# Optimization experiments

Hardware: AMD Instinct MI355X
Metric: run time of the kernel (lower is better)

Reference implementation:

```python
import jax, jax.numpy as jnp
import numpy as np

BLUR = 0.05
P = 2
EPS_FINAL = BLUR ** P          # geomloss: eps = blur**p = 0.0025
DIAMETER = 2.0                 # max cosine cost magnitude
SCALING = 0.5                  # geomloss default; eps decays by scaling**p per step
N_FINAL_ITERS = 4              # extra balancing iterations at the final eps


def eps_schedule():
    eps_list = []
    e = DIAMETER ** P
    while e > EPS_FINAL:
        eps_list.append(e)
        e = e * (SCALING ** P)
    eps_list.extend([EPS_FINAL] * N_FINAL_ITERS)
    return eps_list


def cosine_cost(a, b):
    # a: (N, D), b: (M, D) -> (N, M) cost = 1 - cos_sim
    an = a / (jnp.linalg.norm(a, axis=1, keepdims=True) + 1e-12)
    bn = b / (jnp.linalg.norm(b, axis=1, keepdims=True) + 1e-12)
    return 1.0 - an @ bn.T


def softmin(C, pot, log_w, eps):
    # -eps * LSE_j( log_w + (pot_j - C_ij)/eps ) ; C: (N, M), pot: (M,)
    return -eps * jax.nn.logsumexp(log_w + (pot[None, :] - C) / eps, axis=1)


def sinkhorn_divergence(Cxy, Cxx, Cyy):
    N, M = Cxy.shape
    log_a = -jnp.log(jnp.asarray(N, dtype=Cxy.dtype))  # uniform weights
    log_b = -jnp.log(jnp.asarray(M, dtype=Cxy.dtype))
    sg = jax.lax.stop_gradient
    # Sinkhorn iterations run on detached costs (geomloss envelope-theorem trick)
    Cxy_s, Cxx_s, Cyy_s = sg(Cxy), sg(Cxx), sg(Cyy)
    f = jnp.zeros((N,), Cxy.dtype)
    g = jnp.zeros((M,), Cxy.dtype)
    fxx = jnp.zeros((N,), Cxy.dtype)
    gyy = jnp.zeros((M,), Cxy.dtype)
    for eps in eps_schedule():
        # symmetric (debiasing) potentials: averaged fixed-point update
        fxx = 0.5 * (fxx + softmin(Cxx_s, fxx, log_a, eps))
        gyy = 0.5 * (gyy + softmin(Cyy_s, gyy, log_b, eps))
        # cross potentials: simultaneous (Jacobi) update
        f, g = softmin(Cxy_s, g, log_b, eps), softmin(Cxy_s.T, f, log_a, eps)
    # final extrapolation step with gradients flowing through the costs
    eps = EPS_FINAL
    f_fin = softmin(Cxy, sg(g), log_b, eps)
    g_fin = softmin(Cxy.T, sg(f), log_a, eps)
    fxx_fin = softmin(Cxx, sg(fxx), log_a, eps)
    gyy_fin = softmin(Cyy, sg(gyy), log_b, eps)
    return jnp.mean(f_fin - fxx_fin) + jnp.mean(g_fin - gyy_fin)


def setup_inputs() -> dict:
    key = jax.random.key(0)
    k1, k2, k3 = jax.random.split(key, 3)
    x1 = jax.random.normal(k1, (8192, 256), dtype=jnp.float32)
    x2 = jax.random.normal(k2, (8192, 256), dtype=jnp.float32)
    w = jax.random.uniform(k3, (256,), dtype=jnp.float32)
    return {"x1": x1, "x2": x2, "w": w}


def reference(x1, x2, w):
    # Dist_loss.forward: clamp+renormalize learned per-feature weights, scale x1
    w_c = jnp.clip(w, 0.0, 2.0)
    w_c = w_c / jnp.mean(w_c)
    a = w_c[None, :] * x1
    Cxy = cosine_cost(a, x2)
    Cxx = cosine_cost(a, a)
    Cyy = cosine_cost(x2, x2)
    return sinkhorn_divergence(Cxy, Cxx, Cyy)
```

## Files before the change

### kernel.cpp

```cpp
#include <hip/hip_runtime.h>
#include <math.h>

#define N 8192
#define D 256
#define LN2 0.6931471805599453f
#define LDSROW 280
#define TSLOTS 1152

typedef short short8 __attribute__((ext_vector_type(8)));
typedef float f32x16 __attribute__((ext_vector_type(16)));
typedef unsigned short ushort;

__device__ __forceinline__ float fexp2(float x) { return __builtin_amdgcn_exp2f(x); }
__device__ __forceinline__ float flog2(float x) { return __builtin_amdgcn_logf(x); }

__device__ __forceinline__ ushort bf16r(float x) {
    unsigned int u = __float_as_uint(x);
    return (ushort)((u + 0x7FFF + ((u >> 16) & 1)) >> 16);
}

__device__ __forceinline__ void gl_lds16(const ushort* g, ushort* l) {
    __builtin_amdgcn_global_load_lds(
        (const __attribute__((address_space(1))) unsigned int*)g,
        (__attribute__((address_space(3))) unsigned int*)l, 16, 0, 0);
}

__global__ void prep_wc(const float* __restrict__ w, float* __restrict__ wc) {
    int t = threadIdx.x;
    float v = fminf(fmaxf(w[t], 0.0f), 2.0f);
    float s = v;
#pragma unroll
    for (int m = 1; m < 64; m <<= 1) s += __shfl_xor(s, m);
    __shared__ float sm[4];
    if ((t & 63) == 0) sm[t >> 6] = s;
    __syncthreads();
    float mean = (sm[0] + sm[1] + sm[2] + sm[3]) * (1.0f / 256.0f);
    wc[t] = v / mean;
}

__global__ void prep_normalize(const float* __restrict__ x1, const float* __restrict__ x2,
                               const float* __restrict__ wc,
                               ushort* __restrict__ an_i, ushort* __restrict__ bn_i) {
    int row = blockIdx.x;
    int t = threadIdx.x;
    int r; float v; ushort* ip;
    if (row < N) { r = row;     v = x1[(size_t)r * D + t] * wc[t]; ip = an_i; }
    else         { r = row - N; v = x2[(size_t)r * D + t];         ip = bn_i; }
    float ss = v * v;
#pragma unroll
    for (int m = 1; m < 64; m <<= 1) ss += __shfl_xor(ss, m);
    __shared__ float sm[4];
    if ((t & 63) == 0) sm[t >> 6] = ss;
    __syncthreads();
    float denom = sqrtf(sm[0] + sm[1] + sm[2] + sm[3]) + 1e-12f;
    ip[(size_t)r * D + t] = bf16r(v / denom);
}

__global__ void init_pots(float* __restrict__ pots, float* __restrict__ potm1) {
    int id = blockIdx.x * 256 + threadIdx.x;
    pots[id] = 0.0f;
    potm1[id] = -1.0f;
}

__global__ __launch_bounds__(128, 2) void softmin_mfma(
    const ushort* __restrict__ an_i, const ushort* __restrict__ bn_i,
    const float* __restrict__ potm1,
    float2* __restrict__ parts, float k1) {
    int bx = blockIdx.x;
    int k = bx & 7;
    int q = bx >> 3;
    int task = k >> 1;
    int split = ((k & 1) << 1) | (q >> 6);
    int rb = q & 63;
    const ushort* jp = (task == 0 || task == 3) ? an_i : bn_i;
    const ushort* ip = (task == 0 || task == 2) ? an_i : bn_i;
    const float* pm1 = potm1 + (size_t)task * N;

    int t = threadIdx.x;
    int wave = t >> 6, lane = t & 63;
    int l31 = lane & 31, lh = lane >> 5;
    int i0 = rb * 128 + wave * 64;

    __shared__ ushort lbuf[2][TSLOTS * 8];

    short8 bi0[16], bi1[16];
    {
        const ushort* ib = ip + (size_t)(i0 + l31) * D + lh * 8;
#pragma unroll
        for (int c = 0; c < 16; ++c) {
            bi0[c] = *(const short8*)(ib + c * 16);
            bi1[c] = *(const short8*)(ib + (size_t)32 * D + c * 16);
        }
    }
#pragma unroll
    for (int c = 0; c < 16; ++c) {
        asm volatile("" : "+a"(bi0[c]), "+a"(bi1[c]));
    }

    const int jbase0 = split * 2048;

    int offA[9];
    int offP = 0;
    bool tail = false;
#pragma unroll
    for (int r = 0; r < 9; ++r) {
        int s = r * 128 + t;
        if (s >= 1120) {
            int u = s - 1120;
            offP = (u > 7 ? 7 : u) * 8;
            tail = true;
            offA[r] = 0;
        } else {
            int row = s / 35;
            int c = s - row * 35;
            c = c > 31 ? 31 : c;
            offA[r] = row * D + c * 8;
        }
    }

    auto stage = [&](int b, int js) {
        int j0 = jbase0 + js * 32;
        const ushort* gb = jp + (size_t)j0 * D;
        const ushort* gp = (const ushort*)(pm1 + j0);
        ushort* lb = &lbuf[b][0];
#pragma unroll
        for (int r = 0; r < 8; ++r)
            gl_lds16(gb + offA[r], lb + (r * 128 + t) * 8);
        gl_lds16(tail ? gp + offP : gb + offA[8], lb + (1024 + t) * 8);
    };

    auto tile = [&](const ushort* lb, f32x16& c0, f32x16& c1) {
        const float* pl = (const float*)(lb + 1120 * 8);
        float4 p0 = *(const float4*)&pl[4 * lh + 0];
        float4 p1 = *(const float4*)&pl[4 * lh + 8];
        float4 p2 = *(const float4*)&pl[4 * lh + 16];
        float4 p3 = *(const float4*)&pl[4 * lh + 24];
        c0[0] = p0.x; c0[1] = p0.y; c0[2]  = p0.z; c0[3]  = p0.w;
        c0[4] = p1.x; c0[5] = p1.y; c0[6]  = p1.z; c0[7]  = p1.w;
        c0[8] = p2.x; c0[9] = p2.y; c0[10] = p2.z; c0[11] = p2.w;
        c0[12] = p3.x; c0[13] = p3.y; c0[14] = p3.z; c0[15] = p3.w;
        c1 = c0;
        const ushort* lrow = lb + l31 * LDSROW + lh * 8;
        __builtin_amdgcn_s_setprio(1);
#pragma unroll
        for (int c = 0; c < 16; ++c) {
            short8 af = *(const short8*)(lrow + c * 16);
            c0 = __builtin_amdgcn_mfma_f32_32x32x16_bf16(af, bi0[c], c0, 0, 0, 0);
            c1 = __builtin_amdgcn_mfma_f32_32x32x16_bf16(af, bi1[c], c1, 0, 0, 0);
        }
        __builtin_amdgcn_s_setprio(0);
    };

    float m0 = -INFINITY, s0 = 0.0f, m1 = -INFINITY, s1 = 0.0f;

    auto lse = [&](const f32x16& c, float& m, float& s) {
        float a01 = fmaxf(c[0], c[1]),   a23 = fmaxf(c[2], c[3]);
        float a45 = fmaxf(c[4], c[5]),   a67 = fmaxf(c[6], c[7]);
        float a89 = fmaxf(c[8], c[9]),   aab = fmaxf(c[10], c[11]);
        float acd = fmaxf(c[12], c[13]), aef = fmaxf(c[14], c[15]);
        float q0 = fmaxf(a01, a23), q1 = fmaxf(a45, a67);
        float q2 = fmaxf(a89, aab), q3 = fmaxf(acd, aef);
        float mx = fmaxf(fmaxf(q0, q1), fmaxf(q2, q3));
        float mn = fmaxf(m, mx * k1);
        float nm = -mn;
        float t0 = fexp2(fmaf(c[0],  k1, nm)) + fexp2(fmaf(c[1],  k1, nm));
        float t1 = fexp2(fmaf(c[2],  k1, nm)) + fexp2(fmaf(c[3],  k1, nm));
        float t2 = fexp2(fmaf(c[4],  k1, nm)) + fexp2(fmaf(c[5],  k1, nm));
        float t3 = fexp2(fmaf(c[6],  k1, nm)) + fexp2(fmaf(c[7],  k1, nm));
        float t4 = fexp2(fmaf(c[8],  k1, nm)) + fexp2(fmaf(c[9],  k1, nm));
        float t5 = fexp2(fmaf(c[10], k1, nm)) + fexp2(fmaf(c[11], k1, nm));
        float t6 = fexp2(fmaf(c[12], k1, nm)) + fexp2(fmaf(c[13], k1, nm));
        float t7 = fexp2(fmaf(c[14], k1, nm)) + fexp2(fmaf(c[15], k1, nm));
        float ad = ((t0 + t1) + (t2 + t3)) + ((t4 + t5) + (t6 + t7));
        s = fmaf(s, fexp2(m - mn), ad);
        m = mn;
    };

    f32x16 a0, a1;

    stage(0, 0);
    for (int js = 0; js < 64; ++js) {
        int cur = js & 1;
        __syncthreads();
        if (js < 63) stage(cur ^ 1, js + 1);
        tile(&lbuf[cur][0], a0, a1);
        lse(a0, m0, s0);
        lse(a1, m1, s1);
    }

    float mo = __shfl_xor(m0, 32), so = __shfl_xor(s0, 32);
    float M0 = fmaxf(m0, mo);
    float S0 = s0 * fexp2(m0 - M0) + so * fexp2(mo - M0);
    mo = __shfl_xor(m1, 32); so = __shfl_xor(s1, 32);
    float M1 = fmaxf(m1, mo);
    float S1 = s1 * fexp2(m1 - M1) + so * fexp2(mo - M1);
    if (lane < 32) {
        size_t r0 = (size_t)task * N + (i0 + l31);
        size_t r1 = r0 + 32;
        parts[r0 * 4 + split] = make_float2(M0, S0);
        parts[r1 * 4 + split] = make_float2(M1, S1);
    }
}

__global__ void merge_pots(const float2* __restrict__ parts, float* __restrict__ pots,
                           float* __restrict__ potm1, float eps, float logw, int do_avg) {
    int id = blockIdx.x * 256 + threadIdx.x;
    int task = id >> 13;
    int row = id & (N - 1);
    const float2* p = parts + (size_t)id * 4;
    float2 a = p[0], b = p[1], c = p[2], d = p[3];
    float M = fmaxf(fmaxf(a.x, b.x), fmaxf(c.x, d.x));
    float S = a.y * fexp2(a.x - M) + b.y * fexp2(b.x - M) +
              c.y * fexp2(c.x - M) + d.y * fexp2(d.x - M);
    float lse = LN2 * (M + flog2(S));
    float v = -eps * (logw + lse);
    if (do_avg && task < 2) v = 0.5f * (pots[id] + v);
    pots[id] = v;
    int ct = (task < 2) ? task : (5 - task);
    potm1[(size_t)ct * N + row] = v - 1.0f;
}

__global__ void final_reduce(const float* __restrict__ pots, float* __restrict__ out) {
    int t = threadIdx.x;
    float s = 0.0f;
    for (int i = t; i < N; i += 256)
        s += (pots[2 * N + i] - pots[i]) + (pots[3 * N + i] - pots[N + i]);
#pragma unroll
    for (int m = 1; m < 64; m <<= 1) s += __shfl_xor(s, m);
    __shared__ float sm[4];
    if ((t & 63) == 0) sm[t >> 6] = s;
    __syncthreads();
    if (t == 0) out[0] = (sm[0] + sm[1] + sm[2] + sm[3]) * (1.0f / (float)N);
}

extern "C" void kernel_launch(void* const* d_in, const int* in_sizes, int n_in,
                              void* d_out, int out_size, void* d_ws, size_t ws_size,
                              hipStream_t stream) {
    const float* x1 = (const float*)d_in[0];
    const float* x2 = (const float*)d_in[1];
    const float* w  = (const float*)d_in[2];
    float* out = (float*)d_out;

    ushort* an_i = (ushort*)d_ws;
    ushort* bn_i = an_i + (size_t)N * D;
    float*  wc   = (float*)(bn_i + (size_t)N * D);
    float*  pots = wc + 256;
    float*  potm1 = pots + 4 * N;
    float2* parts = (float2*)(potm1 + 4 * N);

    prep_wc<<<1, 256, 0, stream>>>(w, wc);
    prep_normalize<<<2 * N, 256, 0, stream>>>(x1, x2, wc, an_i, bn_i);
    init_pots<<<4 * N / 256, 256, 0, stream>>>(pots, potm1);

    const float eps_list[10] = {4.0f, 1.0f, 0.25f, 0.0625f, 0.015625f,
                                0.00390625f, 0.0025f, 0.0025f, 0.0025f, 0.0025f};
    const float logw = -logf((float)N);
    const float LOG2E = 1.4426950408889634f;
    for (int it = 0; it < 10; ++it) {
        softmin_mfma<<<1024, 128, 0, stream>>>(an_i, bn_i, potm1, parts, LOG2E / eps_list[it]);
        merge_pots<<<4 * N / 256, 256, 0, stream>>>(parts, pots, potm1,
                                                    eps_list[it], logw, 1);
    }
    softmin_mfma<<<1024, 128, 0, stream>>>(an_i, bn_i, potm1, parts, LOG2E / 0.0025f);
    merge_pots<<<4 * N / 256, 256, 0, stream>>>(parts, pots, potm1, 0.0025f, logw, 0);
    final_reduce<<<1, 256, 0, stream>>>(pots, out);
}
```

Baseline: 1.683 ms.

## Enlarge softmin blocks to 512 threads and 64-column LDS tiles

The fused softmin kernel now uses 8 waves per block covering 512 query rows, with fewer blocks. It stages 64 key columns per step instead of 32, so the loop runs 32 iterations with four MFMA chains per step. Each LDS-staged key tile is shared by more waves and barrier count drops, cutting global-to-LDS traffic per FLOP. In exchange, LDS use per block doubles, the grid shrinks to 256 blocks, and register pressure rises from the extra accumulators.

```diff
diff --git a/kernel.cpp b/kernel.cpp
--- a/kernel.cpp
+++ b/kernel.cpp
@@ -5,7 +5,7 @@
 #define D 256
 #define LN2 0.6931471805599453f
 #define LDSROW 280
-#define TSLOTS 1152
+#define TSLOTS 2304
 
 typedef short short8 __attribute__((ext_vector_type(8)));
 typedef float f32x16 __attribute__((ext_vector_type(16)));
@@ -62,7 +62,7 @@
     potm1[id] = -1.0f;
 }
 
-__global__ __launch_bounds__(128, 2) void softmin_mfma(
+__global__ __launch_bounds__(512, 2) void softmin_mfma(
     const ushort* __restrict__ an_i, const ushort* __restrict__ bn_i,
     const float* __restrict__ potm1,
     float2* __restrict__ parts, float k1) {
@@ -70,8 +70,8 @@
     int k = bx & 7;
     int q = bx >> 3;
     int task = k >> 1;
-    int split = ((k & 1) << 1) | (q >> 6);
-    int rb = q & 63;
+    int split = ((k & 1) << 1) | (q >> 4);
+    int rb = q & 15;
     const ushort* jp = (task == 0 || task == 3) ? an_i : bn_i;
     const ushort* ip = (task == 0 || task == 2) ? an_i : bn_i;
     const float* pm1 = potm1 + (size_t)task * N;
@@ -79,7 +79,7 @@
     int t = threadIdx.x;
     int wave = t >> 6, lane = t & 63;
     int l31 = lane & 31, lh = lane >> 5;
-    int i0 = rb * 128 + wave * 64;
+    int i0 = rb * 512 + wave * 64;
 
     __shared__ ushort lbuf[2][TSLOTS * 8];
 
@@ -99,15 +99,15 @@
 
     const int jbase0 = split * 2048;
 
-    int offA[9];
+    int offA[5];
     int offP = 0;
     bool tail = false;
 #pragma unroll
-    for (int r = 0; r < 9; ++r) {
-        int s = r * 128 + t;
-        if (s >= 1120) {
-            int u = s - 1120;
-            offP = (u > 7 ? 7 : u) * 8;
+    for (int r = 0; r < 5; ++r) {
+        int s = (r < 4) ? (r * 512 + t) : (2048 + t);
+        if (s >= 2240) {
+            int u = s - 2240;
+            offP = (u > 15 ? 15 : u) * 8;
             tail = true;
             offA[r] = 0;
         } else {
@@ -119,36 +119,16 @@
     }
 
     auto stage = [&](int b, int js) {
-        int j0 = jbase0 + js * 32;
+        int j0 = jbase0 + js * 64;
         const ushort* gb = jp + (size_t)j0 * D;
         const ushort* gp = (const ushort*)(pm1 + j0);
         ushort* lb = &lbuf[b][0];
-#pragma unroll
-        for (int r = 0; r < 8; ++r)
-            gl_lds16(gb + offA[r], lb + (r * 128 + t) * 8);
-        gl_lds16(tail ? gp + offP : gb + offA[8], lb + (1024 + t) * 8);
-    };
-
-    auto tile = [&](const ushort* lb, f32x16& c0, f32x16& c1) {
-        const float* pl = (const float*)(lb + 1120 * 8);
-        float4 p0 = *(const float4*)&pl[4 * lh + 0];
-        float4 p1 = *(const float4*)&pl[4 * lh + 8];
-        float4 p2 = *(const float4*)&pl[4 * lh + 16];
-        float4 p3 = *(const float4*)&pl[4 * lh + 24];
-        c0[0] = p0.x; c0[1] = p0.y; c0[2]  = p0.z; c0[3]  = p0.w;
-        c0[4] = p1.x; c0[5] = p1.y; c0[6]  = p1.z; c0[7]  = p1.w;
-        c0[8] = p2.x; c0[9] = p2.y; c0[10] = p2.z; c0[11] = p2.w;
-        c0[12] = p3.x; c0[13] = p3.y; c0[14] = p3.z; c0[15] = p3.w;
-        c1 = c0;
-        const ushort* lrow = lb + l31 * LDSROW + lh * 8;
-        __builtin_amdgcn_s_setprio(1);
-#pragma unroll
-        for (int c = 0; c < 16; ++c) {
-            short8 af = *(const short8*)(lrow + c * 16);
-            c0 = __builtin_amdgcn_mfma_f32_32x32x16_bf16(af, bi0[c], c0, 0, 0, 0);
-            c1 = __builtin_amdgcn_mfma_f32_32x32x16_bf16(af, bi1[c], c1, 0, 0, 0);
-        }
-        __builtin_amdgcn_s_setprio(0);
+        gl_lds16(gb + offA[0], lb + t * 8);
+        gl_lds16(gb + offA[1], lb + (512 + t) * 8);
+        gl_lds16(gb + offA[2], lb + (1024 + t) * 8);
+        gl_lds16(gb + offA[3], lb + (1536 + t) * 8);
+        if (t < 256)
+            gl_lds16(tail ? gp + offP : gb + offA[4], lb + (2048 + t) * 8);
     };
 
     float m0 = -INFINITY, s0 = 0.0f, m1 = -INFINITY, s1 = 0.0f;
@@ -176,16 +156,56 @@
         m = mn;
     };
 
-    f32x16 a0, a1;
+    auto tile64 = [&](const ushort* lb) {
+        const float* pl = (const float*)(lb + 2240 * 8);
+        f32x16 c0, c1, d0, d1;
+        {
+            float4 p0 = *(const float4*)&pl[4 * lh + 0];
+            float4 p1 = *(const float4*)&pl[4 * lh + 8];
+            float4 p2 = *(const float4*)&pl[4 * lh + 16];
+            float4 p3 = *(const float4*)&pl[4 * lh + 24];
+            c0[0] = p0.x; c0[1] = p0.y; c0[2]  = p0.z; c0[3]  = p0.w;
+            c0[4] = p1.x; c0[5] = p1.y; c0[6]  = p1.z; c0[7]  = p1.w;
+            c0[8] = p2.x; c0[9] = p2.y; c0[10] = p2.z; c0[11] = p2.w;
+            c0[12] = p3.x; c0[13] = p3.y; c0[14] = p3.z; c0[15] = p3.w;
+        }
+        c1 = c0;
+        {
+            float4 p0 = *(const float4*)&pl[32 + 4 * lh + 0];
+            float4 p1 = *(const float4*)&pl[32 + 4 * lh + 8];
+            float4 p2 = *(const float4*)&pl[32 + 4 * lh + 16];
+            float4 p3 = *(const float4*)&pl[32 + 4 * lh + 24];
+            d0[0] = p0.x; d0[1] = p0.y; d0[2]  = p0.z; d0[3]  = p0.w;
+            d0[4] = p1.x; d0[5] = p1.y; d0[6]  = p1.z; d0[7]  = p1.w;
+            d0[8] = p2.x; d0[9] = p2.y; d0[10] = p2.z; d0[11] = p2.w;
+            d0[12] = p3.x; d0[13] = p3.y; d0[14] = p3.z; d0[15] = p3.w;
+        }
+        d1 = d0;
+        const ushort* lrow = lb + l31 * LDSROW + lh * 8;
+        const ushort* hrow = lrow + 32 * LDSROW;
+        __builtin_amdgcn_s_setprio(1);
+#pragma unroll
+        for (int c = 0; c < 16; ++c) {
+            short8 alo = *(const short8*)(lrow + c * 16);
+            short8 ahi = *(const short8*)(hrow + c * 16);
+            c0 = __builtin_amdgcn_mfma_f32_32x32x16_bf16(alo, bi0[c], c0, 0, 0, 0);
+            c1 = __builtin_amdgcn_mfma_f32_32x32x16_bf16(alo, bi1[c], c1, 0, 0, 0);
+            d0 = __builtin_amdgcn_mfma_f32_32x32x16_bf16(ahi, bi0[c], d0, 0, 0, 0);
+            d1 = __builtin_amdgcn_mfma_f32_32x32x16_bf16(ahi, bi1[c], d1, 0, 0, 0);
+        }
+        __builtin_amdgcn_s_setprio(0);
+        lse(c0, m0, s0);
+        lse(d0, m0, s0);
+        lse(c1, m1, s1);
+        lse(d1, m1, s1);
+    };
 
     stage(0, 0);
-    for (int js = 0; js < 64; ++js) {
+    for (int js = 0; js < 32; ++js) {
         int cur = js & 1;
         __syncthreads();
-        if (js < 63) stage(cur ^ 1, js + 1);
-        tile(&lbuf[cur][0], a0, a1);
-        lse(a0, m0, s0);
-        lse(a1, m1, s1);
+        if (js < 31) stage(cur ^ 1, js + 1);
+        tile64(&lbuf[cur][0]);
     }
 
     float mo = __shfl_xor(m0, 32), so = __shfl_xor(s0, 32);
@@ -257,11 +277,11 @@
     const float logw = -logf((float)N);
     const float LOG2E = 1.4426950408889634f;
     for (int it = 0; it < 10; ++it) {
-        softmin_mfma<<<1024, 128, 0, stream>>>(an_i, bn_i, potm1, parts, LOG2E / eps_list[it]);
+        softmin_mfma<<<256, 512, 0, stream>>>(an_i, bn_i, potm1, parts, LOG2E / eps_list[it]);
         merge_pots<<<4 * N / 256, 256, 0, stream>>>(parts, pots, potm1,
                                                     eps_list[it], logw, 1);
     }
-    softmin_mfma<<<1024, 128, 0, stream>>>(an_i, bn_i, potm1, parts, LOG2E / 0.0025f);
+    softmin_mfma<<<256, 512, 0, stream>>>(an_i, bn_i, potm1, parts, LOG2E / 0.0025f);
     merge_pots<<<4 * N / 256, 256, 0, stream>>>(parts, pots, potm1, 0.0025f, logw, 0);
     final_reduce<<<1, 256, 0, stream>>>(pots, out);
 }
```

After: 1.513 ms. 1.11x faster.
